# Performance work log

Measured on AMD Instinct MI355X. Metric: run time of the kernel, lower is better.

The kernel has to match this reference:

```python
import jax, jax.numpy as jnp
import numpy as np

EMBED = 1024
HEADS = 16
HEAD_DIM = EMBED // HEADS

def setup_inputs() -> dict:
    key = jax.random.key(0)
    ks = jax.random.split(key, 12)
    N, L, E = 4, 2048, EMBED
    s = 1.0 / np.sqrt(E)
    return {
        "values": jax.random.normal(ks[0], (N, L, E), jnp.float32),
        "keys": jax.random.normal(ks[1], (N, L, E), jnp.float32),
        "query": jax.random.normal(ks[2], (N, L, E), jnp.float32),
        "mask": jnp.ones((N, 1, 1, L), jnp.int32),
        "Wv": jax.random.normal(ks[3], (E, E), jnp.float32) * s,
        "bv": jnp.zeros((E,), jnp.float32),
        "Wk": jax.random.normal(ks[4], (E, E), jnp.float32) * s,
        "bk": jnp.zeros((E,), jnp.float32),
        "Wq": jax.random.normal(ks[5], (E, E), jnp.float32) * s,
        "bq": jnp.zeros((E,), jnp.float32),
        "Wo": jax.random.normal(ks[6], (E, E), jnp.float32) * s,
        "bo": jnp.zeros((E,), jnp.float32),
    }

def reference(values, keys, query, mask, Wv, bv, Wk, bk, Wq, bq, Wo, bo):
    N, L, E = values.shape
    H, D = HEADS, HEAD_DIM
    v = (values @ Wv + bv).reshape(N, L, H, D)
    k = (keys @ Wk + bk).reshape(N, L, H, D)
    q = (query @ Wq + bq).reshape(N, L, H, D)
    # energy: [N, H, Lq, Lk]
    energy = jnp.einsum('nqhd,nkhd->nhqk', q, k)
    energy = jnp.where(mask == 0, jnp.float32(-1e20), energy)
    attn = jax.nn.softmax(energy / np.sqrt(D), axis=3)
    out = jnp.einsum('nhqk,nkhd->nqhd', attn, v).reshape(N, L, E)
    return out @ Wo + bo
```

## Files before the change

### kernel.cpp

```cpp
#include <hip/hip_runtime.h>
#include <hip/hip_bf16.h>


#define N_B 4
#define L_S 2048
#define E_D 1024
#define H_N 16
#define D_H 64

typedef __attribute__((ext_vector_type(8))) short short8;
typedef __attribute__((ext_vector_type(8))) unsigned short ushort8;
typedef __attribute__((ext_vector_type(4))) unsigned short ushort4v;
typedef __attribute__((ext_vector_type(4))) float f32x4;
typedef __attribute__((ext_vector_type(16))) float f32x16;
typedef __attribute__((ext_vector_type(4))) unsigned int uint4v;
typedef __attribute__((ext_vector_type(2))) unsigned int uint2v;

#define EXP2F(x) __builtin_amdgcn_exp2f(x)

__device__ __forceinline__ unsigned short f2b(float f) {
    unsigned int u = __builtin_bit_cast(unsigned int, f);
    u += 0x7fffu + ((u >> 16) & 1u);
    return (unsigned short)(u >> 16);
}

__device__ __forceinline__ void gload16(const void* g, void* l) {
    __builtin_amdgcn_global_load_lds(
        (const __attribute__((address_space(1))) void*)g,
        (__attribute__((address_space(3))) void*)l, 16, 0, 0);
}

__device__ __forceinline__ unsigned int cvtpk(float a, float b) {
    unsigned int w;
    asm("v_cvt_pk_bf16_f32 %0, %1, %2" : "=v"(w) : "v"(a), "v"(b));
    return w;
}

__global__ __launch_bounds__(256) void wtrans4_kernel(const float* __restrict__ W0,
                                                      const float* __restrict__ W1,
                                                      const float* __restrict__ W2,
                                                      const float* __restrict__ W3,
                                                      unsigned short* __restrict__ WtBase) {
    __shared__ float t[64][65];
    int z = blockIdx.z;
    const float* W = (z == 0) ? W0 : ((z == 1) ? W1 : ((z == 2) ? W2 : W3));
    unsigned short* Wt = WtBase + (size_t)z * (1u << 20);
    int bx = blockIdx.x, by = blockIdx.y;
    int tx = threadIdx.x;
    int r0 = tx >> 4;
    int c4 = (tx & 15) << 2;
#pragma unroll
    for (int rr = 0; rr < 64; rr += 16) {
        const float* src = W + (size_t)(by * 64 + rr + r0) * E_D + bx * 64 + c4;
        float4 v = *(const float4*)src;
        t[rr + r0][c4 + 0] = v.x; t[rr + r0][c4 + 1] = v.y;
        t[rr + r0][c4 + 2] = v.z; t[rr + r0][c4 + 3] = v.w;
    }
    __syncthreads();
#pragma unroll
    for (int rr = 0; rr < 64; rr += 16) {
        int nrow = bx * 64 + rr + r0;
        ushort4v o;
#pragma unroll
        for (int j = 0; j < 4; j++) o[j] = f2b(t[c4 + j][rr + r0]);
        *(ushort4v*)(Wt + (size_t)nrow * E_D + by * 64 + c4) = o;
    }
}

__device__ __forceinline__ void gemm_body_bf16a(
    const unsigned short* __restrict__ A, const unsigned short* __restrict__ Bt,
    const float* __restrict__ bias, float* __restrict__ C,
    int K, int Nc, float scale,
    unsigned short* As, unsigned short* Bs, int n0, int m0) {
    int lane = threadIdx.x & 63, wave = threadIdx.x >> 6;
    int wr = (wave >> 1) * 64, wc = (wave & 1) * 64;
    f32x4 acc[4][4] = {};
    int nk = K >> 6;
    for (int kt = 0; kt < nk; ++kt) {
#pragma unroll
        for (int i = 0; i < 4; i++) {
            int c = (i * 4 + wave) * 64 + lane;
            int row = c >> 3;
            int csw = (c & 7) ^ (row & 7);
            gload16(A + (size_t)(m0 + row) * K + kt * 64 + csw * 8,
                    As + (size_t)(i * 4 + wave) * 512);
            gload16(Bt + (size_t)(n0 + row) * K + kt * 64 + csw * 8,
                    Bs + (size_t)(i * 4 + wave) * 512);
        }
        __syncthreads();
#pragma unroll
        for (int ks = 0; ks < 2; ++ks) {
            short8 a[4], b[4];
#pragma unroll
            for (int mi = 0; mi < 4; mi++) {
                int row = wr + mi * 16 + (lane & 15);
                int ch = (ks * 4 + (lane >> 4)) ^ (row & 7);
                a[mi] = *(const short8*)(As + row * 64 + ch * 8);
            }
#pragma unroll
            for (int ni = 0; ni < 4; ni++) {
                int col = wc + ni * 16 + (lane & 15);
                int ch = (ks * 4 + (lane >> 4)) ^ (col & 7);
                b[ni] = *(const short8*)(Bs + col * 64 + ch * 8);
            }
#pragma unroll
            for (int mi = 0; mi < 4; mi++)
#pragma unroll
                for (int ni = 0; ni < 4; ni++)
                    acc[mi][ni] = __builtin_amdgcn_mfma_f32_16x16x32_bf16(
                        a[mi], b[ni], acc[mi][ni], 0, 0, 0);
        }
        __syncthreads();
    }
#pragma unroll
    for (int ni = 0; ni < 4; ni++) {
        int col = n0 + wc + ni * 16 + (lane & 15);
        float bb = bias[col];
#pragma unroll
        for (int mi = 0; mi < 4; mi++) {
            int rbase = m0 + wr + mi * 16 + (lane >> 4) * 4;
#pragma unroll
            for (int r = 0; r < 4; r++)
                C[(size_t)(rbase + r) * Nc + col] = (acc[mi][ni][r] + bb) * scale;
        }
    }
}

__global__ __launch_bounds__(256, 2) void gemm_out_kernel(
    const unsigned short* __restrict__ A, const unsigned short* __restrict__ Bt,
    const float* __restrict__ bias, float* __restrict__ C,
    int M, int K, int Nc, float scale) {
    __shared__ unsigned short SMEM[2][128 * 64];
    gemm_body_bf16a(A, Bt, bias, C, K, Nc, scale, SMEM[0], SMEM[1],
                    blockIdx.x * 128, blockIdx.y * 128);
}

template <int OUTMODE>
__device__ __forceinline__ void gemm_body_f32a(
    const float* __restrict__ A, const unsigned short* __restrict__ Bt,
    const float* __restrict__ bias, unsigned short* __restrict__ C,
    float scale, float* AsF, unsigned short* Bs, int n0, int m0) {
    int lane = threadIdx.x & 63, wave = threadIdx.x >> 6;
    int wr = (wave >> 1) * 64, wc = (wave & 1) * 64;
    f32x4 acc[4][4] = {};
    for (int kt = 0; kt < E_D / 64; ++kt) {
#pragma unroll
        for (int i = 0; i < 8; i++) {
            int cc = (i * 4 + wave) * 64 + lane;
            int row = cc >> 4;
            int csw = (cc & 15) ^ (row & 15);
            gload16(A + (size_t)(m0 + row) * E_D + kt * 64 + csw * 4,
                    AsF + (size_t)(i * 4 + wave) * 256);
        }
#pragma unroll
        for (int i = 0; i < 4; i++) {
            int cc = (i * 4 + wave) * 64 + lane;
            int row = cc >> 3;
            int csw = (cc & 7) ^ (row & 7);
            gload16(Bt + (size_t)(n0 + row) * E_D + kt * 64 + csw * 8,
                    Bs + (size_t)(i * 4 + wave) * 512);
        }
        __syncthreads();
#pragma unroll
        for (int ks = 0; ks < 2; ++ks) {
            short8 a[4], b[4];
#pragma unroll
            for (int mi = 0; mi < 4; mi++) {
                int row = wr + mi * 16 + (lane & 15);
                int c16 = ks * 8 + (lane >> 4) * 2;
                int p0 = c16 ^ (row & 15);
                int p1 = (c16 + 1) ^ (row & 15);
                f32x4 f0 = *(const f32x4*)(AsF + row * 64 + p0 * 4);
                f32x4 f1 = *(const f32x4*)(AsF + row * 64 + p1 * 4);
                uint4v ua;
                ua[0] = cvtpk(f0[0], f0[1]); ua[1] = cvtpk(f0[2], f0[3]);
                ua[2] = cvtpk(f1[0], f1[1]); ua[3] = cvtpk(f1[2], f1[3]);
                a[mi] = __builtin_bit_cast(short8, ua);
            }
#pragma unroll
            for (int ni = 0; ni < 4; ni++) {
                int col = wc + ni * 16 + (lane & 15);
                int ch = (ks * 4 + (lane >> 4)) ^ (col & 7);
                b[ni] = *(const short8*)(Bs + col * 64 + ch * 8);
            }
#pragma unroll
            for (int mi = 0; mi < 4; mi++)
#pragma unroll
                for (int ni = 0; ni < 4; ni++)
                    acc[mi][ni] = __builtin_amdgcn_mfma_f32_16x16x32_bf16(
                        a[mi], b[ni], acc[mi][ni], 0, 0, 0);
        }
        __syncthreads();
    }
    if (OUTMODE == 2) {
        int g = lane >> 4, c = lane & 15;
        unsigned short* tb = (unsigned short*)AsF + wave * 4096;
#pragma unroll
        for (int ni = 0; ni < 4; ni++) {
            int cl = ni * 16 + c;
            float bb = bias[n0 + wc + cl];
#pragma unroll
            for (int mi = 0; mi < 4; mi++) {
#pragma unroll
                for (int r = 0; r < 4; r++) {
                    int rl = mi * 16 + g * 4 + r;
                    tb[rl * 64 + (((cl >> 3) ^ (rl & 7)) << 3) + (cl & 7)] =
                        f2b((acc[mi][ni][r] + bb) * scale);
                }
            }
        }
        int mrow = m0 + wr;
        int n = mrow >> 11;
        int l0 = mrow & 2047;
        int h = (n0 + wc) >> 6;
#pragma unroll
        for (int i = 0; i < 8; i++) {
            int d = i * 8 + (lane >> 3);
            int lc = (lane & 7) * 8;
            ushort8 ov;
#pragma unroll
            for (int j = 0; j < 8; j++) {
                int rl = lc + j;
                ov[j] = tb[rl * 64 + (((d >> 3) ^ (rl & 7)) << 3) + (d & 7)];
            }
            *(ushort8*)(C + (size_t)((n * H_N + h) * D_H + d) * L_S + l0 + lc) = ov;
        }
        return;
    }
#pragma unroll
    for (int ni = 0; ni < 4; ni++) {
        int col = n0 + wc + ni * 16 + (lane & 15);
        float bb = bias[col];
#pragma unroll
        for (int mi = 0; mi < 4; mi++) {
            int rbase = m0 + wr + mi * 16 + (lane >> 4) * 4;
#pragma unroll
            for (int r = 0; r < 4; r++)
                C[(size_t)(rbase + r) * E_D + col] = f2b((acc[mi][ni][r] + bb) * scale);
        }
    }
}

__global__ __launch_bounds__(256, 2) void gemm3_kernel(
    const float* __restrict__ Vf, const float* __restrict__ Kf, const float* __restrict__ Qf,
    const unsigned short* __restrict__ Wtbase,
    const float* __restrict__ bv, const float* __restrict__ bk, const float* __restrict__ bq,
    unsigned short* __restrict__ vT, unsigned short* __restrict__ kbf,
    unsigned short* __restrict__ qbf, float qscale) {
    __shared__ float AsF[128 * 64];
    __shared__ unsigned short Bs[128 * 64];
    int z = blockIdx.z;
    const unsigned short* Bt = Wtbase + (size_t)z * (1u << 20);
    int m0 = blockIdx.x * 128, n0 = blockIdx.y * 128;
    if (z == 0) {
        gemm_body_f32a<2>(Vf, Bt, bv, vT, 1.0f, AsF, Bs, n0, m0);
    } else if (z == 1) {
        gemm_body_f32a<0>(Kf, Bt, bk, kbf, 1.0f, AsF, Bs, n0, m0);
    } else {
        gemm_body_f32a<0>(Qf, Bt, bq, qbf, qscale, AsF, Bs, n0, m0);
    }
}

__global__ __launch_bounds__(512, 4) void attn_kernel(
    const unsigned short* __restrict__ qb, const unsigned short* __restrict__ kb,
    const unsigned short* __restrict__ vt, const int* __restrict__ mask,
    unsigned short* __restrict__ aout) {
    __shared__ unsigned short KV[4][64 * 64];
    __shared__ alignas(8) unsigned char okb[256];
    int lane = threadIdx.x & 63, wave = threadIdx.x >> 6;
    int qc = lane & 31, hl = lane >> 5;

    int bid = blockIdx.x;
    int xcd = bid & 7, idx = bid >> 3;
    int grp = xcd * 8 + (idx >> 3);
    int q0 = (idx & 7) * 256;
    int hd = grp & 15;
    int n = grp >> 4;

    const unsigned short* qptr  = qb + (size_t)n * L_S * E_D + hd * 64;
    const unsigned short* kbase = kb + (size_t)n * L_S * E_D + hd * 64;
    const unsigned short* vbase = vt + (size_t)(n * H_N + hd) * D_H * L_S;
    const int* mbase = mask + n * L_S;

    if (threadIdx.x < 256) {
        int t8 = threadIdx.x * 8;
        int4 ma = *(const int4*)(mbase + t8);
        int4 mb = *(const int4*)(mbase + t8 + 4);
        int ok = (ma.x != 0) & (ma.y != 0) & (ma.z != 0) & (ma.w != 0) &
                 (mb.x != 0) & (mb.y != 0) & (mb.z != 0) & (mb.w != 0);
        okb[threadIdx.x] = (unsigned char)ok;
    }
    unsigned short* Qs = &KV[0][0];
#pragma unroll
    for (int i = 0; i < 4; i++) {
        gload16(qptr + (size_t)(q0 + wave * 32 + (lane & 31)) * E_D + (2 * i + (lane >> 5)) * 8,
                Qs + wave * 2048 + i * 512);
    }
    __syncthreads();
    short8 qf[4];
#pragma unroll
    for (int dk = 0; dk < 4; dk++)
        qf[dk] = *(const short8*)(Qs + wave * 2048 + (dk * 2 + hl) * 256 + qc * 8);
    __syncthreads();
    gload16(kbase + (size_t)lane * E_D + wave * 8, KV[0] + wave * 512);
    gload16(vbase + (size_t)lane * L_S + wave * 8, KV[2] + wave * 512);

    f32x16 o[2] = {};
    float lrun = 0.f;

    const int NT = L_S / 64;
    for (int kt = 0; kt < NT; ++kt) {
        int cur = kt & 1;
        asm volatile("s_waitcnt vmcnt(0)" ::: "memory");
        __builtin_amdgcn_s_barrier();
        __builtin_amdgcn_sched_barrier(0);
        if (kt + 1 < NT) {
            gload16(kbase + (size_t)((kt + 1) * 64 + lane) * E_D + wave * 8,
                    KV[cur ^ 1] + wave * 512);
            gload16(vbase + (size_t)lane * L_S + (kt + 1) * 64 + wave * 8,
                    KV[2 + (cur ^ 1)] + wave * 512);
        }

        const unsigned short* KsC = KV[cur];
        const unsigned short* VsC = KV[2 + cur];

        f32x16 sT0 = {}, sT1 = {};
        __builtin_amdgcn_s_setprio(1);
#pragma unroll
        for (int dk = 0; dk < 4; dk++) {
            int ch = (dk * 2 + hl) * 512;
            short8 kf0 = *(const short8*)(KsC + ch + qc * 8);
            short8 kf1 = *(const short8*)(KsC + ch + (32 + qc) * 8);
            sT0 = __builtin_amdgcn_mfma_f32_32x32x16_bf16(kf0, qf[dk], sT0, 0, 0, 0);
            sT1 = __builtin_amdgcn_mfma_f32_32x32x16_bf16(kf1, qf[dk], sT1, 0, 0, 0);
        }
        __builtin_amdgcn_s_setprio(0);

        uint2 fl = *(const uint2*)&okb[kt * 8];
        bool dense = ((fl.x & fl.y) == 0x01010101u);
        if (!dense) {
#pragma unroll
            for (int reg = 0; reg < 16; reg++) {
                int crow = (reg & 3) + 8 * (reg >> 2) + 4 * hl;
                int key = kt * 64 + crow;
                sT0[reg] += mbase[key] ? 0.f : -1e30f;
                sT1[reg] += mbase[key + 32] ? 0.f : -1e30f;
            }
        }
        float ps = 0.f;
#pragma unroll
        for (int kg = 0; kg < 2; kg++) {
            const f32x16& sS = (kg == 0) ? sT0 : sT1;
            float p[16];
#pragma unroll
            for (int r = 0; r < 16; r++) {
                p[r] = EXP2F(sS[r]);
                ps += p[r];
            }
            unsigned int w[8];
#pragma unroll
            for (int a = 0; a < 8; a++) w[a] = cvtpk(p[2 * a], p[2 * a + 1]);
            uint2v r02 = __builtin_amdgcn_permlane32_swap(w[0], w[2], false, false);
            uint2v r13 = __builtin_amdgcn_permlane32_swap(w[1], w[3], false, false);
            uint2v r46 = __builtin_amdgcn_permlane32_swap(w[4], w[6], false, false);
            uint2v r57 = __builtin_amdgcn_permlane32_swap(w[5], w[7], false, false);
            uint4v u0, u1;
            u0[0] = r02.x; u0[1] = r13.x; u0[2] = r02.y; u0[3] = r13.y;
            u1[0] = r46.x; u1[1] = r57.x; u1[2] = r46.y; u1[3] = r57.y;
            short8 pa0 = __builtin_bit_cast(short8, u0);
            short8 pa1 = __builtin_bit_cast(short8, u1);
            __builtin_amdgcn_s_setprio(1);
#pragma unroll
            for (int dg = 0; dg < 2; dg++) {
                int vr = dg * 32 + qc;
                short8 vb0 = *(const short8*)(VsC + (kg * 4 + hl) * 512 + vr * 8);
                short8 vb1 = *(const short8*)(VsC + (kg * 4 + 2 + hl) * 512 + vr * 8);
                o[dg] = __builtin_amdgcn_mfma_f32_32x32x16_bf16(pa0, vb0, o[dg], 0, 0, 0);
                o[dg] = __builtin_amdgcn_mfma_f32_32x32x16_bf16(pa1, vb1, o[dg], 0, 0, 0);
            }
            __builtin_amdgcn_s_setprio(0);
        }
        ps += __shfl_xor(ps, 32);
        lrun += ps;
    }
#pragma unroll
    for (int reg = 0; reg < 16; reg++) {
        int crow = (reg & 3) + 8 * (reg >> 2) + 4 * hl;
        float iv = 1.f / __shfl(lrun, crow);
        size_t rb = (size_t)(n * L_S + q0 + wave * 32 + crow) * E_D + hd * 64 + qc;
        aout[rb]      = f2b(o[0][reg] * iv);
        aout[rb + 32] = f2b(o[1][reg] * iv);
    }
}

extern "C" void kernel_launch(void* const* d_in, const int* in_sizes, int n_in,
                              void* d_out, int out_size, void* d_ws, size_t ws_size,
                              hipStream_t stream) {
    const float* values = (const float*)d_in[0];
    const float* keys   = (const float*)d_in[1];
    const float* query  = (const float*)d_in[2];
    const int*   mask   = (const int*)d_in[3];
    const float* Wv = (const float*)d_in[4];  const float* bv = (const float*)d_in[5];
    const float* Wk = (const float*)d_in[6];  const float* bk = (const float*)d_in[7];
    const float* Wq = (const float*)d_in[8];  const float* bq = (const float*)d_in[9];
    const float* Wo = (const float*)d_in[10]; const float* bo = (const float*)d_in[11];
    float* out = (float*)d_out;
    char* ws = (char*)d_ws;
    const size_t MB = 1ull << 20;
    unsigned short* wtv = (unsigned short*)(ws + 48 * MB);
    unsigned short* wto = (unsigned short*)(ws + 54 * MB);
    unsigned short* vT  = (unsigned short*)(ws + 56 * MB);
    unsigned short* kbf = (unsigned short*)(ws + 72 * MB);
    unsigned short* qbf = (unsigned short*)(ws + 88 * MB);
    unsigned short* aob = (unsigned short*)(ws + 16 * MB);

    const float QS = 0.125f * 1.4426950408889634f;

    wtrans4_kernel<<<dim3(16, 16, 4), 256, 0, stream>>>(Wv, Wk, Wq, Wo, wtv);
    gemm3_kernel<<<dim3((N_B * L_S) / 128, E_D / 128, 3), 256, 0, stream>>>(
        values, keys, query, wtv, bv, bk, bq, vT, kbf, qbf, QS);
    attn_kernel<<<dim3(512), 512, 0, stream>>>(qbf, kbf, vT, mask, aob);
    gemm_out_kernel<<<dim3(E_D / 128, (N_B * L_S) / 128), 256, 0, stream>>>(
        aob, wto, bo, out, N_B * L_S, E_D, E_D, 1.0f);
}
```

Baseline: 192.0 us.

## Prefetch QKV projection tiles into registers and store bf16 A tile in LDS

```diff
diff --git a/kernel.cpp b/kernel.cpp
--- a/kernel.cpp
+++ b/kernel.cpp
@@ -139,26 +139,51 @@
 __device__ __forceinline__ void gemm_body_f32a(
     const float* __restrict__ A, const unsigned short* __restrict__ Bt,
     const float* __restrict__ bias, unsigned short* __restrict__ C,
-    float scale, float* AsF, unsigned short* Bs, int n0, int m0) {
+    float scale, unsigned short* As, unsigned short* Bs, int n0, int m0) {
     int lane = threadIdx.x & 63, wave = threadIdx.x >> 6;
     int wr = (wave >> 1) * 64, wc = (wave & 1) * 64;
     f32x4 acc[4][4] = {};
-    for (int kt = 0; kt < E_D / 64; ++kt) {
-#pragma unroll
-        for (int i = 0; i < 8; i++) {
-            int cc = (i * 4 + wave) * 64 + lane;
-            int row = cc >> 4;
-            int csw = (cc & 15) ^ (row & 15);
-            gload16(A + (size_t)(m0 + row) * E_D + kt * 64 + csw * 4,
-                    AsF + (size_t)(i * 4 + wave) * 256);
-        }
+
+    int crow[4], ccsw[4], coff[4];
+#pragma unroll
+    for (int i = 0; i < 4; i++) {
+        int cc = (i * 4 + wave) * 64 + lane;
+        crow[i] = cc >> 3;
+        ccsw[i] = (cc & 7) ^ (crow[i] & 7);
+        coff[i] = cc * 8;
+    }
+
+    f32x4 ar[4][2];
+    ushort8 br[4];
+#pragma unroll
+    for (int i = 0; i < 4; i++) {
+        const float* ap = A + (size_t)(m0 + crow[i]) * E_D + ccsw[i] * 8;
+        ar[i][0] = *(const f32x4*)ap;
+        ar[i][1] = *(const f32x4*)(ap + 4);
+        br[i] = *(const ushort8*)(Bt + (size_t)(n0 + crow[i]) * E_D + ccsw[i] * 8);
+    }
+
+    const int nk = E_D / 64;
+    for (int kt = 0; kt < nk; ++kt) {
+        __syncthreads();
 #pragma unroll
         for (int i = 0; i < 4; i++) {
-            int cc = (i * 4 + wave) * 64 + lane;
-            int row = cc >> 3;
-            int csw = (cc & 7) ^ (row & 7);
-            gload16(Bt + (size_t)(n0 + row) * E_D + kt * 64 + csw * 8,
-                    Bs + (size_t)(i * 4 + wave) * 512);
+            uint4v u;
+            u[0] = cvtpk(ar[i][0][0], ar[i][0][1]);
+            u[1] = cvtpk(ar[i][0][2], ar[i][0][3]);
+            u[2] = cvtpk(ar[i][1][0], ar[i][1][1]);
+            u[3] = cvtpk(ar[i][1][2], ar[i][1][3]);
+            *(ushort8*)(As + coff[i]) = __builtin_bit_cast(ushort8, u);
+            *(ushort8*)(Bs + coff[i]) = br[i];
+        }
+        if (kt + 1 < nk) {
+#pragma unroll
+            for (int i = 0; i < 4; i++) {
+                const float* ap = A + (size_t)(m0 + crow[i]) * E_D + (kt + 1) * 64 + ccsw[i] * 8;
+                ar[i][0] = *(const f32x4*)ap;
+                ar[i][1] = *(const f32x4*)(ap + 4);
+                br[i] = *(const ushort8*)(Bt + (size_t)(n0 + crow[i]) * E_D + (kt + 1) * 64 + ccsw[i] * 8);
+            }
         }
         __syncthreads();
 #pragma unroll
@@ -167,15 +192,8 @@
 #pragma unroll
             for (int mi = 0; mi < 4; mi++) {
                 int row = wr + mi * 16 + (lane & 15);
-                int c16 = ks * 8 + (lane >> 4) * 2;
-                int p0 = c16 ^ (row & 15);
-                int p1 = (c16 + 1) ^ (row & 15);
-                f32x4 f0 = *(const f32x4*)(AsF + row * 64 + p0 * 4);
-                f32x4 f1 = *(const f32x4*)(AsF + row * 64 + p1 * 4);
-                uint4v ua;
-                ua[0] = cvtpk(f0[0], f0[1]); ua[1] = cvtpk(f0[2], f0[3]);
-                ua[2] = cvtpk(f1[0], f1[1]); ua[3] = cvtpk(f1[2], f1[3]);
-                a[mi] = __builtin_bit_cast(short8, ua);
+                int ch = (ks * 4 + (lane >> 4)) ^ (row & 7);
+                a[mi] = *(const short8*)(As + row * 64 + ch * 8);
             }
 #pragma unroll
             for (int ni = 0; ni < 4; ni++) {
@@ -190,11 +208,11 @@
                     acc[mi][ni] = __builtin_amdgcn_mfma_f32_16x16x32_bf16(
                         a[mi], b[ni], acc[mi][ni], 0, 0, 0);
         }
+    }
+    if (OUTMODE == 2) {
         __syncthreads();
-    }
-    if (OUTMODE == 2) {
         int g = lane >> 4, c = lane & 15;
-        unsigned short* tb = (unsigned short*)AsF + wave * 4096;
+        unsigned short* tb = As + wave * 4096;
 #pragma unroll
         for (int ni = 0; ni < 4; ni++) {
             int cl = ni * 16 + c;
@@ -241,23 +259,22 @@
     }
 }
 
-__global__ __launch_bounds__(256, 2) void gemm3_kernel(
+__global__ __launch_bounds__(256, 3) void gemm3_kernel(
     const float* __restrict__ Vf, const float* __restrict__ Kf, const float* __restrict__ Qf,
     const unsigned short* __restrict__ Wtbase,
     const float* __restrict__ bv, const float* __restrict__ bk, const float* __restrict__ bq,
     unsigned short* __restrict__ vT, unsigned short* __restrict__ kbf,
     unsigned short* __restrict__ qbf, float qscale) {
-    __shared__ float AsF[128 * 64];
-    __shared__ unsigned short Bs[128 * 64];
+    __shared__ unsigned short SMEM[2][128 * 64];
     int z = blockIdx.z;
     const unsigned short* Bt = Wtbase + (size_t)z * (1u << 20);
     int m0 = blockIdx.x * 128, n0 = blockIdx.y * 128;
     if (z == 0) {
-        gemm_body_f32a<2>(Vf, Bt, bv, vT, 1.0f, AsF, Bs, n0, m0);
+        gemm_body_f32a<2>(Vf, Bt, bv, vT, 1.0f, SMEM[0], SMEM[1], n0, m0);
     } else if (z == 1) {
-        gemm_body_f32a<0>(Kf, Bt, bk, kbf, 1.0f, AsF, Bs, n0, m0);
+        gemm_body_f32a<0>(Kf, Bt, bk, kbf, 1.0f, SMEM[0], SMEM[1], n0, m0);
     } else {
-        gemm_body_f32a<0>(Qf, Bt, bq, qbf, qscale, AsF, Bs, n0, m0);
+        gemm_body_f32a<0>(Qf, Bt, bq, qbf, qscale, SMEM[0], SMEM[1], n0, m0);
     }
 }
 
```

Result: faster. 186.5 us (-2.9%).
